# Kernel tuning notes

Hardware: AMD Instinct MI355X
Metric: run time of the kernel (lower is better)

## Reference

```python
import jax, jax.numpy as jnp
import numpy as np

N_EMBD = 1024
N_HEAD = 16
D_HEAD = N_EMBD // N_HEAD


def setup_inputs() -> dict:
    key = jax.random.key(0)
    ks = jax.random.split(key, 5)
    x = jax.random.normal(ks[0], (4, 2048, N_EMBD), dtype=jnp.float32)
    s = 1.0 / np.sqrt(N_EMBD)
    Wq = jax.random.normal(ks[1], (N_EMBD, N_EMBD), dtype=jnp.float32) * s
    Wk = jax.random.normal(ks[2], (N_EMBD, N_EMBD), dtype=jnp.float32) * s
    Wv = jax.random.normal(ks[3], (N_EMBD, N_EMBD), dtype=jnp.float32) * s
    Wo = jax.random.normal(ks[4], (N_EMBD, N_EMBD), dtype=jnp.float32) * s
    return {"x": x, "Wq": Wq, "Wk": Wk, "Wv": Wv, "Wo": Wo}


def reference(x, Wq, Wk, Wv, Wo):
    B, S, E = x.shape
    H, Dh = N_HEAD, D_HEAD
    scale = 1.0 / np.sqrt(Dh)  # LayerwiseSDPA(d_head) -> scale by 1/sqrt(d_head)

    def proj(W):
        # nn.Linear(no bias): y = x @ W.T ; reshape to [B,H,S,Dh]
        return (x @ W.T).reshape(B, S, H, Dh).transpose(0, 2, 1, 3)

    q, k, v = proj(Wq), proj(Wk), proj(Wv)
    scores = jnp.einsum('bhsd,bhtd->bhst', q, k) * scale  # [B,H,S,S]
    causal = jnp.tril(jnp.ones((S, S), dtype=bool))
    scores = jnp.where(causal, scores, jnp.finfo(scores.dtype).min)
    attn = jax.nn.softmax(scores, axis=-1)
    y = jnp.einsum('bhst,bhtd->bhsd', attn, v)  # [B,H,S,Dh]
    y = y.transpose(0, 2, 1, 3).reshape(B, S, E)
    return y @ Wo.T
```

## Files before the change

### kernel.cpp

```cpp
#include <hip/hip_runtime.h>

typedef __bf16 bf16;
typedef bf16  bf16x8 __attribute__((ext_vector_type(8)));
typedef bf16  bf16x4 __attribute__((ext_vector_type(4)));
typedef short s16x4  __attribute__((ext_vector_type(4)));
typedef float f32x4  __attribute__((ext_vector_type(4)));

#define AS1 __attribute__((address_space(1)))
#define AS3 __attribute__((address_space(3)))

#define SQLEN 2048
#define EMB   1024

__global__ __launch_bounds__(256) void cvt_f32_bf16(const float* __restrict__ in,
                                                    bf16* __restrict__ out, int n8) {
  int i = blockIdx.x * blockDim.x + threadIdx.x;
  if (i >= n8) return;
  const float4* p = (const float4*)in + (size_t)i * 2;
  float4 a = p[0], b = p[1];
  bf16x8 o;
  o[0] = (bf16)a.x; o[1] = (bf16)a.y; o[2] = (bf16)a.z; o[3] = (bf16)a.w;
  o[4] = (bf16)b.x; o[5] = (bf16)b.y; o[6] = (bf16)b.z; o[7] = (bf16)b.w;
  *((bf16x8*)out + i) = o;
}

__global__ __launch_bounds__(256) void cvt_w4(const float* __restrict__ w0, const float* __restrict__ w1,
                                              const float* __restrict__ w2, const float* __restrict__ w3,
                                              bf16* o0, bf16* o1, bf16* o2, bf16* o3, int n8) {
  const float* in; bf16* out;
  switch (blockIdx.y) {
    case 0: in = w0; out = o0; break;
    case 1: in = w1; out = o1; break;
    case 2: in = w2; out = o2; break;
    default: in = w3; out = o3; break;
  }
  int i = blockIdx.x * blockDim.x + threadIdx.x;
  if (i >= n8) return;
  const float4* p = (const float4*)in + (size_t)i * 2;
  float4 a = p[0], b = p[1];
  bf16x8 o;
  o[0] = (bf16)a.x; o[1] = (bf16)a.y; o[2] = (bf16)a.z; o[3] = (bf16)a.w;
  o[4] = (bf16)b.x; o[5] = (bf16)b.y; o[6] = (bf16)b.z; o[7] = (bf16)b.w;
  *((bf16x8*)out + i) = o;
}

template <int OUTF32>
__device__ __forceinline__
void gemm_body(const bf16* __restrict__ A, const bf16* __restrict__ B,
               float* __restrict__ Cf, bf16* __restrict__ Cb,
               int M, int N, int K, float scale, bf16* Asl, bf16* Bsl, int vtr) {
  const int tid  = threadIdx.x;
  const int lane = tid & 63, wave = tid >> 6;
  const int quad = lane >> 4, col = lane & 15;
  const int m0 = blockIdx.x * 128, n0 = blockIdx.y * 128;
  const int wr = wave >> 1, wc = wave & 1;

  f32x4 acc[4][4];
  const f32x4 fz = {0.f, 0.f, 0.f, 0.f};
#pragma unroll
  for (int i = 0; i < 4; ++i)
#pragma unroll
    for (int j = 0; j < 4; ++j) acc[i][j] = fz;

  const int srow = lane >> 2;
  const int sk   = lane & 3;

  auto stage = [&](int buf, int k0) {
#pragma unroll
    for (int r = 0; r < 2; ++r) {
      const int c      = wave * 2 + r;
      const int row    = c * 16 + srow;
      const int gchunk = sk ^ (row & 3);
      const bf16* ga = A + (size_t)(m0 + row) * K + k0 + gchunk * 8;
      const bf16* gb = B + (size_t)(n0 + row) * K + k0 + gchunk * 8;
      __builtin_amdgcn_global_load_lds((const AS1 void*)ga, (AS3 void*)(Asl + buf * 4096 + c * 512), 16, 0, 0);
      __builtin_amdgcn_global_load_lds((const AS1 void*)gb, (AS3 void*)(Bsl + buf * 4096 + c * 512), 16, 0, 0);
    }
  };

  const int nk = K >> 5;
  stage(0, 0);
  for (int it = 0; it < nk; ++it) {
    __syncthreads();
    if (it + 1 < nk) stage((it + 1) & 1, (it + 1) << 5);
    const bf16* As = Asl + (it & 1) * 4096;
    const bf16* Bs = Bsl + (it & 1) * 4096;

    bf16x8 af[4], bfr[4];
#pragma unroll
    for (int i = 0; i < 4; ++i) {
      const int r = wr * 64 + i * 16 + col;
      af[i] = *(const bf16x8*)&As[r * 32 + ((quad ^ (col & 3)) * 8)];
    }
#pragma unroll
    for (int j = 0; j < 4; ++j) {
      const int r = wc * 64 + j * 16 + col;
      bfr[j] = *(const bf16x8*)&Bs[r * 32 + ((quad ^ (col & 3)) * 8)];
    }
#pragma unroll
    for (int i = 0; i < 4; ++i)
#pragma unroll
      for (int j = 0; j < 4; ++j)
        acc[i][j] = __builtin_amdgcn_mfma_f32_16x16x32_bf16(af[i], bfr[j], acc[i][j], 0, 0, 0);
  }

#pragma unroll
  for (int i = 0; i < 4; ++i) {
#pragma unroll
    for (int j = 0; j < 4; ++j) {
      const int gm0 = m0 + wr * 64 + i * 16 + quad * 4;
      const int gn  = n0 + wc * 64 + j * 16 + col;
      if (OUTF32) {
#pragma unroll
        for (int r = 0; r < 4; ++r)
          Cf[(size_t)(gm0 + r) * N + gn] = acc[i][j][r] * scale;
      } else if (vtr) {
        bf16x4 ob;
#pragma unroll
        for (int r = 0; r < 4; ++r) ob[r] = (bf16)(acc[i][j][r] * scale);
        const int bb = gm0 >> 11;
        const int t_ = gm0 & 2047;
        *(bf16x4*)&Cb[((size_t)(bb * 1024 + gn)) * 2048 + t_] = ob;
      } else {
#pragma unroll
        for (int r = 0; r < 4; ++r)
          Cb[(size_t)(gm0 + r) * N + gn] = (bf16)(acc[i][j][r] * scale);
      }
    }
  }
}

__global__ __launch_bounds__(256, 2)
void gemm_qkv(const bf16* __restrict__ A, const bf16* __restrict__ Wq,
              const bf16* __restrict__ Wk, const bf16* __restrict__ Wv,
              bf16* Qo, bf16* Ko, bf16* Vto, float qscale) {
  __shared__ bf16 Asl[2 * 4096];
  __shared__ bf16 Bsl[2 * 4096];
  const bf16* B; bf16* C; float sc = 1.0f; int vtr = 0;
  if (blockIdx.z == 0)      { B = Wq; C = Qo; sc = qscale; }
  else if (blockIdx.z == 1) { B = Wk; C = Ko; }
  else                      { B = Wv; C = Vto; vtr = 1; }
  gemm_body<0>(A, B, nullptr, C, 8192, 1024, 1024, sc, Asl, Bsl, vtr);
}

__global__ __launch_bounds__(256, 2)
void gemm_o(const bf16* __restrict__ A, const bf16* __restrict__ W, float* __restrict__ C) {
  __shared__ bf16 Asl[2 * 4096];
  __shared__ bf16 Bsl[2 * 4096];
  gemm_body<1>(A, W, C, nullptr, 8192, 1024, 1024, 1.0f, Asl, Bsl, 0);
}

__global__ __launch_bounds__(512, 4)
void attn_flash(const bf16* __restrict__ Q, const bf16* __restrict__ K,
                const bf16* __restrict__ Vt, bf16* __restrict__ Y) {
  __shared__ bf16 Ksb0[2 * 8192];
  __shared__ bf16 Vsb0[2 * 8192];

  const int tid  = threadIdx.x;
  const int lane = tid & 63, wave = tid >> 6;
  const int quad = lane >> 4, col = lane & 15;

  const int B_ = blockIdx.x;
  const int bh = (B_ & 7) * 8 + (B_ >> 6);
  const int p  = (B_ >> 3) & 7;
  const int h  = bh & 15;
  const int b  = bh >> 4;
  const int hc = h * 64;
  const size_t rowBase = (size_t)b * SQLEN;

  const int srow8 = lane >> 3;
  const int sch   = lane & 7;
  const int a7    = col & 7;

  auto stageKV = [&](int buf, int t0) {
#pragma unroll
    for (int i = 0; i < 2; ++i) {
      const int krow = wave * 16 + i * 8 + srow8;
      const int kch  = sch ^ srow8;
      const bf16* gk = K + (rowBase + t0 + krow) * EMB + hc + kch * 8;
      __builtin_amdgcn_global_load_lds((const AS1 void*)gk,
          (AS3 void*)(Ksb0 + buf * 8192 + wave * 1024 + i * 512), 16, 0, 0);
      const int vrow = wave * 8 + i * 4 + (lane >> 4);
      const int vch  = (lane & 15) ^ (vrow & 7);
      const bf16* gv = Vt + ((size_t)(b * EMB + hc + vrow)) * SQLEN + t0 + vch * 8;
      __builtin_amdgcn_global_load_lds((const AS1 void*)gv,
          (AS3 void*)(Vsb0 + buf * 8192 + wave * 1024 + i * 512), 16, 0, 0);
    }
  };

  const s16x4 ones = {(short)0x3F80, (short)0x3F80, (short)0x3F80, (short)0x3F80};

  for (int halfIdx = 0; halfIdx < 2; ++halfIdx) {
    const int qt = halfIdx == 0 ? (15 - p) : p;
    const int q0 = qt * 128;
    const int ntt = qt + 1;

    stageKV(0, 0);

    bf16x8 qf0, qf1;
    {
      const int row = wave * 16 + col;
      const bf16* gq = Q + (rowBase + q0 + row) * EMB + hc + quad * 8;
      qf0 = *(const bf16x8*)gq;
      qf1 = *(const bf16x8*)(gq + 32);
    }
    __syncthreads();

    float m_i = -INFINITY;
    f32x4 o[4], ol;
    const f32x4 fz = {0.f, 0.f, 0.f, 0.f};
#pragma unroll
    for (int dd = 0; dd < 4; ++dd) o[dd] = fz;
    ol = fz;

    for (int tt = 0; tt < ntt; ++tt) {
      const int t0 = tt * 128;
      const int cur = tt & 1;
      if (tt + 1 < ntt) stageKV(cur ^ 1, t0 + 128);
      const bf16* Ks = Ksb0 + cur * 8192;
      const bf16* Vs = Vsb0 + cur * 8192;

      f32x4 s[8];
      __builtin_amdgcn_s_setprio(1);
#pragma unroll
      for (int sl = 0; sl < 8; ++sl) {
        const bf16x8 kf0 = *(const bf16x8*)&Ks[(sl * 16 + col) * 64 + ((quad ^ a7) * 8)];
        const bf16x8 kf1 = *(const bf16x8*)&Ks[(sl * 16 + col) * 64 + (((quad ^ 4) ^ a7) * 8)];
        f32x4 z = fz;
        z = __builtin_amdgcn_mfma_f32_16x16x32_bf16(kf0, qf0, z, 0, 0, 0);
        s[sl] = __builtin_amdgcn_mfma_f32_16x16x32_bf16(kf1, qf1, z, 0, 0, 0);
      }
      __builtin_amdgcn_s_setprio(0);

      if (tt == qt) {
        const int qg = q0 + wave * 16 + col;
#pragma unroll
        for (int sl = 0; sl < 8; ++sl)
#pragma unroll
          for (int r = 0; r < 4; ++r)
            if (t0 + sl * 16 + quad * 4 + r > qg) s[sl][r] = -INFINITY;
      }

      bf16x4 pb[8];
      {
        float mx = s[0][0];
#pragma unroll
        for (int sl = 0; sl < 8; ++sl)
#pragma unroll
          for (int r = 0; r < 4; ++r) mx = fmaxf(mx, s[sl][r]);
        mx = fmaxf(mx, __shfl_xor(mx, 16));
        mx = fmaxf(mx, __shfl_xor(mx, 32));
        if (!__all(mx <= m_i + 8.f)) {
          const float mnew = fmaxf(m_i, mx);
          const float a = __builtin_amdgcn_exp2f(m_i - mnew);
#pragma unroll
          for (int dd = 0; dd < 4; ++dd) o[dd] *= a;
          ol *= a;
          m_i = mnew;
        }
#pragma unroll
        for (int sl = 0; sl < 8; ++sl)
#pragma unroll
          for (int r = 0; r < 4; ++r)
            pb[sl][r] = (bf16)__builtin_amdgcn_exp2f(s[sl][r] - m_i);
      }

      __builtin_amdgcn_s_setprio(1);
#pragma unroll
      for (int sl = 0; sl < 8; ++sl) {
        const s16x4 pf = __builtin_bit_cast(s16x4, pb[sl]);
        ol = __builtin_amdgcn_mfma_f32_16x16x16bf16_1k(ones, pf, ol, 0, 0, 0);
        const int cch  = 2 * sl + (quad >> 1);
        const int half = quad & 1;
#pragma unroll
        for (int dd = 0; dd < 4; ++dd) {
          const int row = dd * 16 + col;
          const bf16x4 vb = *(const bf16x4*)&Vs[row * 128 + ((cch ^ a7) * 8) + half * 4];
          const s16x4 vf = __builtin_bit_cast(s16x4, vb);
          o[dd] = __builtin_amdgcn_mfma_f32_16x16x16bf16_1k(vf, pf, o[dd], 0, 0, 0);
        }
      }
      __builtin_amdgcn_s_setprio(0);
      __syncthreads();
    }

    {
      const float rl = __builtin_amdgcn_rcpf(ol[0]);
      const size_t yrow = (rowBase + q0 + wave * 16 + col) * EMB + hc;
#pragma unroll
      for (int dd = 0; dd < 4; ++dd) {
        bf16x4 ob;
#pragma unroll
        for (int r = 0; r < 4; ++r) ob[r] = (bf16)(o[dd][r] * rl);
        *(bf16x4*)&Y[yrow + dd * 16 + quad * 4] = ob;
      }
    }
  }
}

extern "C" void kernel_launch(void* const* d_in, const int* in_sizes, int n_in,
                              void* d_out, int out_size, void* d_ws, size_t ws_size,
                              hipStream_t stream) {
  const float* x  = (const float*)d_in[0];
  const float* Wq = (const float*)d_in[1];
  const float* Wk = (const float*)d_in[2];
  const float* Wv = (const float*)d_in[3];
  const float* Wo = (const float*)d_in[4];
  float* out = (float*)d_out;

  const size_t ME = 8192ull * 1024ull;
  const size_t WE = 1024ull * 1024ull;
  bf16* ws  = (bf16*)d_ws;
  bf16* xb  = ws;
  bf16* wqb = xb + ME;
  bf16* wkb = wqb + WE;
  bf16* wvb = wkb + WE;
  bf16* wob = wvb + WE;
  bf16* Qb  = wob + WE;
  bf16* Kb  = Qb + ME;
  bf16* Vtb = Kb + ME;
  bf16* Yb  = Vtb + ME;

  cvt_f32_bf16<<<(int)(ME / 8 / 256), 256, 0, stream>>>(x, xb, (int)(ME / 8));
  cvt_w4<<<dim3((int)(WE / 8 / 256), 4), 256, 0, stream>>>(Wq, Wk, Wv, Wo, wqb, wkb, wvb, wob, (int)(WE / 8));

  const float qscale = 0.125f * 1.4426950408889634f;
  gemm_qkv<<<dim3(64, 8, 3), 256, 0, stream>>>(xb, wqb, wkb, wvb, Qb, Kb, Vtb, qscale);

  attn_flash<<<512, 512, 0, stream>>>(Qb, Kb, Vtb, Yb);

  gemm_o<<<dim3(64, 8), 256, 0, stream>>>(Yb, wob, out);
}
```

Before: 251.4 us.

## Fuse Q/K/V projections into one GEMM sharing the A tile

Replaces the three-way blockIdx.z split of the QKV projection with a single kernel in which each block computes Q, K and V tiles at once. It loads the x tile once into shared memory per k-step and reuses its fragments across all three weight matrices, cutting redundant A traffic and staging. The cost is three times the accumulator registers (48 f32x4 per thread) and more LDS, with only 512 blocks instead of 1536. Occupancy drops and register spills are possible under launch_bounds(256,2).

```diff
diff --git a/kernel.cpp b/kernel.cpp
--- a/kernel.cpp
+++ b/kernel.cpp
@@ -44,11 +44,10 @@
   *((bf16x8*)out + i) = o;
 }
 
-template <int OUTF32>
 __device__ __forceinline__
-void gemm_body(const bf16* __restrict__ A, const bf16* __restrict__ B,
-               float* __restrict__ Cf, bf16* __restrict__ Cb,
-               int M, int N, int K, float scale, bf16* Asl, bf16* Bsl, int vtr) {
+void gemm_body_f32(const bf16* __restrict__ A, const bf16* __restrict__ B,
+                   float* __restrict__ Cf, int M, int N, int K,
+                   bf16* Asl, bf16* Bsl) {
   const int tid  = threadIdx.x;
   const int lane = tid & 63, wave = tid >> 6;
   const int quad = lane >> 4, col = lane & 15;
@@ -110,22 +109,9 @@
     for (int j = 0; j < 4; ++j) {
       const int gm0 = m0 + wr * 64 + i * 16 + quad * 4;
       const int gn  = n0 + wc * 64 + j * 16 + col;
-      if (OUTF32) {
-#pragma unroll
-        for (int r = 0; r < 4; ++r)
-          Cf[(size_t)(gm0 + r) * N + gn] = acc[i][j][r] * scale;
-      } else if (vtr) {
-        bf16x4 ob;
-#pragma unroll
-        for (int r = 0; r < 4; ++r) ob[r] = (bf16)(acc[i][j][r] * scale);
-        const int bb = gm0 >> 11;
-        const int t_ = gm0 & 2047;
-        *(bf16x4*)&Cb[((size_t)(bb * 1024 + gn)) * 2048 + t_] = ob;
-      } else {
-#pragma unroll
-        for (int r = 0; r < 4; ++r)
-          Cb[(size_t)(gm0 + r) * N + gn] = (bf16)(acc[i][j][r] * scale);
-      }
+#pragma unroll
+      for (int r = 0; r < 4; ++r)
+        Cf[(size_t)(gm0 + r) * N + gn] = acc[i][j][r];
     }
   }
 }
@@ -133,21 +119,112 @@
 __global__ __launch_bounds__(256, 2)
 void gemm_qkv(const bf16* __restrict__ A, const bf16* __restrict__ Wq,
               const bf16* __restrict__ Wk, const bf16* __restrict__ Wv,
-              bf16* Qo, bf16* Ko, bf16* Vto, float qscale) {
+              bf16* __restrict__ Qo, bf16* __restrict__ Ko, bf16* __restrict__ Vto,
+              float qscale) {
   __shared__ bf16 Asl[2 * 4096];
-  __shared__ bf16 Bsl[2 * 4096];
-  const bf16* B; bf16* C; float sc = 1.0f; int vtr = 0;
-  if (blockIdx.z == 0)      { B = Wq; C = Qo; sc = qscale; }
-  else if (blockIdx.z == 1) { B = Wk; C = Ko; }
-  else                      { B = Wv; C = Vto; vtr = 1; }
-  gemm_body<0>(A, B, nullptr, C, 8192, 1024, 1024, sc, Asl, Bsl, vtr);
+  __shared__ bf16 Bsl[3][2 * 4096];
+
+  const int tid  = threadIdx.x;
+  const int lane = tid & 63, wave = tid >> 6;
+  const int quad = lane >> 4, col = lane & 15;
+  const int m0 = blockIdx.x * 128, n0 = blockIdx.y * 128;
+  const int wr = wave >> 1, wc = wave & 1;
+  const int K = 1024, N = 1024;
+
+  const bf16* const Bp[3] = {Wq, Wk, Wv};
+
+  f32x4 acc[3][4][4];
+  const f32x4 fz = {0.f, 0.f, 0.f, 0.f};
+#pragma unroll
+  for (int s = 0; s < 3; ++s)
+#pragma unroll
+    for (int i = 0; i < 4; ++i)
+#pragma unroll
+      for (int j = 0; j < 4; ++j) acc[s][i][j] = fz;
+
+  const int srow = lane >> 2;
+  const int sk   = lane & 3;
+
+  auto stage = [&](int buf, int k0) {
+#pragma unroll
+    for (int r = 0; r < 2; ++r) {
+      const int c      = wave * 2 + r;
+      const int row    = c * 16 + srow;
+      const int gchunk = sk ^ (row & 3);
+      const bf16* ga = A + (size_t)(m0 + row) * K + k0 + gchunk * 8;
+      __builtin_amdgcn_global_load_lds((const AS1 void*)ga,
+          (AS3 void*)(Asl + buf * 4096 + c * 512), 16, 0, 0);
+#pragma unroll
+      for (int s = 0; s < 3; ++s) {
+        const bf16* gb = Bp[s] + (size_t)(n0 + row) * K + k0 + gchunk * 8;
+        __builtin_amdgcn_global_load_lds((const AS1 void*)gb,
+            (AS3 void*)(&Bsl[s][buf * 4096 + c * 512]), 16, 0, 0);
+      }
+    }
+  };
+
+  const int nk = K >> 5;
+  stage(0, 0);
+  for (int it = 0; it < nk; ++it) {
+    __syncthreads();
+    if (it + 1 < nk) stage((it + 1) & 1, (it + 1) << 5);
+    const bf16* As = Asl + (it & 1) * 4096;
+
+    bf16x8 af[4];
+#pragma unroll
+    for (int i = 0; i < 4; ++i) {
+      const int r = wr * 64 + i * 16 + col;
+      af[i] = *(const bf16x8*)&As[r * 32 + ((quad ^ (col & 3)) * 8)];
+    }
+#pragma unroll
+    for (int s = 0; s < 3; ++s) {
+      const bf16* Bs = &Bsl[s][(it & 1) * 4096];
+      bf16x8 bfr[4];
+#pragma unroll
+      for (int j = 0; j < 4; ++j) {
+        const int r = wc * 64 + j * 16 + col;
+        bfr[j] = *(const bf16x8*)&Bs[r * 32 + ((quad ^ (col & 3)) * 8)];
+      }
+#pragma unroll
+      for (int i = 0; i < 4; ++i)
+#pragma unroll
+        for (int j = 0; j < 4; ++j)
+          acc[s][i][j] = __builtin_amdgcn_mfma_f32_16x16x32_bf16(af[i], bfr[j], acc[s][i][j], 0, 0, 0);
+    }
+  }
+
+#pragma unroll
+  for (int s = 0; s < 3; ++s) {
+    const float sc = (s == 0) ? qscale : 1.0f;
+#pragma unroll
+    for (int i = 0; i < 4; ++i) {
+#pragma unroll
+      for (int j = 0; j < 4; ++j) {
+        const int gm0 = m0 + wr * 64 + i * 16 + quad * 4;
+        const int gn  = n0 + wc * 64 + j * 16 + col;
+        if (s == 2) {
+          bf16x4 ob;
+#pragma unroll
+          for (int r = 0; r < 4; ++r) ob[r] = (bf16)(acc[s][i][j][r]);
+          const int bb = gm0 >> 11;
+          const int t_ = gm0 & 2047;
+          *(bf16x4*)&Vto[((size_t)(bb * 1024 + gn)) * 2048 + t_] = ob;
+        } else {
+          bf16* C = (s == 0) ? Qo : Ko;
+#pragma unroll
+          for (int r = 0; r < 4; ++r)
+            C[(size_t)(gm0 + r) * N + gn] = (bf16)(acc[s][i][j][r] * sc);
+        }
+      }
+    }
+  }
 }
 
 __global__ __launch_bounds__(256, 2)
 void gemm_o(const bf16* __restrict__ A, const bf16* __restrict__ W, float* __restrict__ C) {
   __shared__ bf16 Asl[2 * 4096];
   __shared__ bf16 Bsl[2 * 4096];
-  gemm_body<1>(A, W, C, nullptr, 8192, 1024, 1024, 1.0f, Asl, Bsl, 0);
+  gemm_body_f32(A, W, C, 8192, 1024, 1024, Asl, Bsl);
 }
 
 __global__ __launch_bounds__(512, 4)
@@ -325,7 +402,7 @@
   cvt_w4<<<dim3((int)(WE / 8 / 256), 4), 256, 0, stream>>>(Wq, Wk, Wv, Wo, wqb, wkb, wvb, wob, (int)(WE / 8));
 
   const float qscale = 0.125f * 1.4426950408889634f;
-  gemm_qkv<<<dim3(64, 8, 3), 256, 0, stream>>>(xb, wqb, wkb, wvb, Qb, Kb, Vtb, qscale);
+  gemm_qkv<<<dim3(64, 8), 256, 0, stream>>>(xb, wqb, wkb, wvb, Qb, Kb, Vtb, qscale);
 
   attn_flash<<<512, 512, 0, stream>>>(Qb, Kb, Vtb, Yb);
 
```

After: 240.5 us. -4.3%, faster.
